# Performance work log

Measured on AMD Instinct MI355X. Metric: run time of the kernel, lower is better.

## Reference

```python
import jax, jax.numpy as jnp
import numpy as np

D_K = 64
D_MODEL = 1024
SEQ = 4096
BATCH = 4


def setup_inputs() -> dict:
    key = jax.random.key(0)
    ks = jax.random.split(key, 7)
    s = 1.0 / np.sqrt(D_MODEL)
    return {
        "x": jax.random.normal(ks[0], (BATCH, SEQ, D_MODEL), dtype=jnp.float32),
        "wq": jax.random.uniform(ks[1], (D_K, D_MODEL), jnp.float32, -s, s),
        "bq": jax.random.uniform(ks[2], (D_K,), jnp.float32, -s, s),
        "wk": jax.random.uniform(ks[3], (D_K, D_MODEL), jnp.float32, -s, s),
        "bk": jax.random.uniform(ks[4], (D_K,), jnp.float32, -s, s),
        "wv": jax.random.uniform(ks[5], (D_K, D_MODEL), jnp.float32, -s, s),
        "bv": jax.random.uniform(ks[6], (D_K,), jnp.float32, -s, s),
    }


def reference(x, wq, bq, wk, bk, wv, bv):
    # q,k,v: [B,T,d_k]
    q = jnp.einsum('btc,dc->btd', x, wq) + bq
    k = jnp.einsum('btc,dc->btd', x, wk) + bk
    v = jnp.einsum('btc,dc->btd', x, wv) + bv
    scale = 1.0 / np.sqrt(D_K).astype(np.float32)
    scores = jnp.einsum('bqd,bkd->bqk', q, k) * scale  # [B,T,T]
    T = x.shape[1]
    causal = jnp.tril(jnp.ones((T, T), dtype=bool))
    scores = jnp.where(causal, scores, -jnp.inf)
    sm = jax.nn.softmax(scores, axis=-1)
    return jnp.einsum('bqk,bkd->bqd', sm, v)
```

## Files before the change

kernel.cpp:

```cpp
#include <hip/hip_runtime.h>

typedef __attribute__((ext_vector_type(8))) short short8;
typedef __attribute__((ext_vector_type(4))) float f32x4;

#define D_KV   64
#define SEQ    4096
#define NBATCH 4
#define DMODEL 1024

static __device__ __forceinline__ unsigned short f32_to_bf16(float f) {
  unsigned u = __builtin_bit_cast(unsigned, f);
  u = (u + 0x7FFFu + ((u >> 16) & 1u)) >> 16;
  return (unsigned short)u;
}

__global__ __launch_bounds__(256) void xfrag_kernel(
    const float* __restrict__ x, unsigned short* __restrict__ xfrag) {
  __shared__ unsigned short lt[16 * 1024];
  const int tid = threadIdx.x;
  const long T = blockIdx.x;
  {
    const int row = tid >> 4, seg = tid & 15;
    const float* src = x + (T * 16 + row) * DMODEL + seg * 64;
    unsigned short* dst = lt + row * 1024 + seg * 64;
#pragma unroll
    for (int j = 0; j < 8; ++j) {
      const f32x4 f0 = *reinterpret_cast<const f32x4*>(src + j * 8);
      const f32x4 f1 = *reinterpret_cast<const f32x4*>(src + j * 8 + 4);
      short8 s;
#pragma unroll
      for (int q = 0; q < 4; ++q) {
        s[q] = (short)f32_to_bf16(f0[q]);
        s[4 + q] = (short)f32_to_bf16(f1[q]);
      }
      *reinterpret_cast<short8*>(dst + j * 8) = s;
    }
  }
  __syncthreads();
  unsigned short* dst = xfrag + T * 16384;
#pragma unroll
  for (int i = 0; i < 8; ++i) {
    const int slot = i * 256 + tid;
    const int lane2 = slot & 63, ks = slot >> 6;
    const short8 v = *reinterpret_cast<const short8*>(
        lt + (lane2 & 15) * 1024 + ks * 32 + (lane2 >> 4) * 8);
    *reinterpret_cast<short8*>(dst + slot * 8) = v;
  }
}

__global__ __launch_bounds__(256) void wcvt_kernel(
    const float* __restrict__ wq, const float* __restrict__ wk,
    const float* __restrict__ wv, unsigned short* __restrict__ wfrag) {
  const int fid = blockIdx.x * 256 + threadIdx.x;
  const int nt = fid >> 11, ks = (fid >> 6) & 31, lane = fid & 63;
  const int l16 = lane & 15, lq = lane >> 4;
  const float* w = (nt < 4) ? wq : (nt < 8) ? wk : wv;
  const float* src = w + ((nt & 3) * 16 + l16) * DMODEL + ks * 32 + lq * 8;
  short8 v;
#pragma unroll
  for (int j = 0; j < 8; ++j) v[j] = (short)f32_to_bf16(src[j]);
  *reinterpret_cast<short8*>(wfrag + (long)fid * 8) = v;
}

__global__ __launch_bounds__(256, 2) void qkv_proj_kernel(
    const unsigned short* __restrict__ xfrag,
    const unsigned short* __restrict__ wfrag,
    const float* __restrict__ bq, const float* __restrict__ bk,
    const float* __restrict__ bv,
    unsigned short* __restrict__ Qf, unsigned short* __restrict__ Kf,
    unsigned short* __restrict__ Vf) {
  const int tid = threadIdx.x, lane = tid & 63, wave = tid >> 6;
  const int l16 = lane & 15, lq = lane >> 4;
  const long T = blockIdx.x;

  const unsigned short* abase = xfrag + T * 16384 + lane * 8;
  const unsigned short* wbase = wfrag + (long)(3 * wave) * 16384 + lane * 8;

  f32x4 acc[3];
#pragma unroll
  for (int i = 0; i < 3; ++i) acc[i] = (f32x4){0.f, 0.f, 0.f, 0.f};

#pragma unroll
  for (int ck = 0; ck < 8; ++ck) {
    short8 a[4], bw[12];
#pragma unroll
    for (int kc = 0; kc < 4; ++kc)
      a[kc] = *reinterpret_cast<const short8*>(abase + (ck * 4 + kc) * 512);
#pragma unroll
    for (int j = 0; j < 12; ++j)
      bw[j] = *reinterpret_cast<const short8*>(
          wbase + (long)(j >> 2) * 16384 + (ck * 4 + (j & 3)) * 512);
#pragma unroll
    for (int kc = 0; kc < 4; ++kc)
#pragma unroll
      for (int i = 0; i < 3; ++i)
        acc[i] = __builtin_amdgcn_mfma_f32_16x16x32_bf16(
            a[kc], bw[i * 4 + kc], acc[i], 0, 0, 0);
  }

#pragma unroll
  for (int i = 0; i < 3; ++i) {
    const int nt = 3 * wave + i;
    const int mat = nt >> 2;
    const int dcol = ((nt & 3) << 4) | l16;
    const float bias = (mat == 0 ? bq : mat == 1 ? bk : bv)[dcol];
    const int c = dcol >> 5, lqp = (dcol >> 3) & 3, jj = dcol & 7;
#pragma unroll
    for (int rr = 0; rr < 4; ++rr) {
      const long t = T * 16 + lq * 4 + rr;
      const float sum = acc[i][rr] + bias;
      if (mat == 0) {
        Qf[(((t >> 4) * 2 + c) * 64 + lqp * 16 + (t & 15)) * 8 + jj] =
            f32_to_bf16(sum * 0.125f);
      } else if (mat == 1) {
        Kf[((((t >> 6) * 4 + ((t >> 4) & 3)) * 2 + c) * 64 + lqp * 16 +
            (t & 15)) * 8 + jj] = f32_to_bf16(sum);
      } else {
        Vf[((((t >> 6) * 4 + (dcol >> 4)) * 2 + ((t >> 5) & 1)) * 64 +
            ((t >> 3) & 3) * 16 + (dcol & 15)) * 8 + (t & 7)] =
            f32_to_bf16(sum);
      }
    }
  }
}

__global__ __launch_bounds__(256) void attn_kernel(
    const unsigned short* __restrict__ Qf, const unsigned short* __restrict__ Kf,
    const unsigned short* __restrict__ Vf, float* __restrict__ out) {
  __shared__ __align__(16) unsigned short p_lds[4][16][72];
  __shared__ __align__(16) float lds_o[4][16][68];
  __shared__ float lds_ml[4][16][2];
  __shared__ float lds_gl[16];

  const int tid = threadIdx.x;
  const int lane = tid & 63;
  const int wave = tid >> 6;
  const int l16 = lane & 15, lq = lane >> 4;
  const int b = blockIdx.y;
  const int tile = 255 - blockIdx.x;
  const int qbase = tile * 16;
  const long qrow = (long)b * SEQ + qbase;

  short8 qf[2];
#pragma unroll
  for (int c = 0; c < 2; ++c)
    qf[c] = *reinterpret_cast<const short8*>(
        Qf + ((qrow >> 4) * 2 + c) * 512 + lane * 8);

  f32x4 o[4];
#pragma unroll
  for (int dt = 0; dt < 4; ++dt) o[dt] = (f32x4){0.f, 0.f, 0.f, 0.f};
  float m = -INFINITY, ell = 0.f;

  const long ktile0 = (long)b * 64;
  const int nkv = qbase / 64 + 1;
  for (int kt = wave; kt < nkv; kt += 4) {
    const int kvbase = kt * 64;
    const unsigned short* kb = Kf + (ktile0 + kt) * 4096 + lane * 8;
    const unsigned short* vb = Vf + (ktile0 + kt) * 4096 + lane * 8;
    f32x4 s[4];
#pragma unroll
    for (int ct = 0; ct < 4; ++ct) s[ct] = (f32x4){0.f, 0.f, 0.f, 0.f};
#pragma unroll
    for (int ct = 0; ct < 4; ++ct)
#pragma unroll
      for (int c = 0; c < 2; ++c) {
        short8 kf = *reinterpret_cast<const short8*>(kb + (ct * 2 + c) * 512);
        s[ct] = __builtin_amdgcn_mfma_f32_16x16x32_bf16(kf, qf[c], s[ct], 0, 0, 0);
      }
    if (kt == nkv - 1) {
      const int qg = qbase + l16;
#pragma unroll
      for (int ct = 0; ct < 4; ++ct)
#pragma unroll
        for (int r = 0; r < 4; ++r)
          if (kvbase + ct * 16 + lq * 4 + r > qg) s[ct][r] = -INFINITY;
    }
    float mx = -INFINITY;
#pragma unroll
    for (int ct = 0; ct < 4; ++ct)
#pragma unroll
      for (int r = 0; r < 4; ++r) mx = fmaxf(mx, s[ct][r]);
    mx = fmaxf(mx, __shfl_xor(mx, 16, 64));
    mx = fmaxf(mx, __shfl_xor(mx, 32, 64));
    const float nm = fmaxf(m, mx);
    const float alpha = __expf(m - nm);
    float rs = 0.f;
#pragma unroll
    for (int ct = 0; ct < 4; ++ct)
#pragma unroll
      for (int r = 0; r < 4; ++r) {
        const float p = __expf(s[ct][r] - nm);
        s[ct][r] = p;
        rs += p;
      }
    rs += __shfl_xor(rs, 16, 64);
    rs += __shfl_xor(rs, 32, 64);
    ell = ell * alpha + rs;
    m = nm;
#pragma unroll
    for (int dt = 0; dt < 4; ++dt) o[dt] *= alpha;
#pragma unroll
    for (int ct = 0; ct < 4; ++ct)
#pragma unroll
      for (int r = 0; r < 4; ++r)
        p_lds[wave][l16][ct * 16 + lq * 4 + r] = f32_to_bf16(s[ct][r]);
    short8 pf[2];
#pragma unroll
    for (int c = 0; c < 2; ++c)
      pf[c] = *reinterpret_cast<const short8*>(&p_lds[wave][l16][c * 32 + lq * 8]);
#pragma unroll
    for (int dt = 0; dt < 4; ++dt)
#pragma unroll
      for (int c = 0; c < 2; ++c) {
        short8 vf = *reinterpret_cast<const short8*>(vb + (dt * 2 + c) * 512);
        o[dt] = __builtin_amdgcn_mfma_f32_16x16x32_bf16(vf, pf[c], o[dt], 0, 0, 0);
      }
  }

  if (lane < 16) {
    lds_ml[wave][l16][0] = m;
    lds_ml[wave][l16][1] = ell;
  }
  __syncthreads();
  const float m0 = lds_ml[0][l16][0], m1 = lds_ml[1][l16][0];
  const float m2 = lds_ml[2][l16][0], m3 = lds_ml[3][l16][0];
  const float g = fmaxf(fmaxf(m0, m1), fmaxf(m2, m3));
  const float gl = lds_ml[0][l16][1] * __expf(m0 - g) +
                   lds_ml[1][l16][1] * __expf(m1 - g) +
                   lds_ml[2][l16][1] * __expf(m2 - g) +
                   lds_ml[3][l16][1] * __expf(m3 - g);
  const float myscale = __expf(m - g);
  if (wave == 0 && lane < 16) lds_gl[l16] = gl;
#pragma unroll
  for (int dt = 0; dt < 4; ++dt)
#pragma unroll
    for (int r = 0; r < 4; ++r)
      lds_o[wave][l16][dt * 16 + lq * 4 + r] = o[dt][r] * myscale;
  __syncthreads();
#pragma unroll
  for (int j = 0; j < 4; ++j) {
    const int e = tid + 256 * j;
    const int row = e >> 6, col = e & 63;
    const float sum = lds_o[0][row][col] + lds_o[1][row][col] +
                      lds_o[2][row][col] + lds_o[3][row][col];
    out[(qrow + row) * D_KV + col] = sum / lds_gl[row];
  }
}

extern "C" void kernel_launch(void* const* d_in, const int* in_sizes, int n_in,
                              void* d_out, int out_size, void* d_ws, size_t ws_size,
                              hipStream_t stream) {
  const float* x  = (const float*)d_in[0];
  const float* wq = (const float*)d_in[1];
  const float* bq = (const float*)d_in[2];
  const float* wk = (const float*)d_in[3];
  const float* bk = (const float*)d_in[4];
  const float* wv = (const float*)d_in[5];
  const float* bv = (const float*)d_in[6];
  float* out = (float*)d_out;

  unsigned short* ws    = (unsigned short*)d_ws;
  unsigned short* wfrag = ws;
  unsigned short* Qf    = ws + 196608;
  unsigned short* Kf    = Qf + 1048576;
  unsigned short* Vf    = Kf + 1048576;
  unsigned short* xfrag = Vf + 1048576;

  xfrag_kernel<<<1024, 256, 0, stream>>>(x, xfrag);
  wcvt_kernel<<<96, 256, 0, stream>>>(wq, wk, wv, wfrag);
  qkv_proj_kernel<<<1024, 256, 0, stream>>>(xfrag, wfrag, bq, bk, bv, Qf, Kf, Vf);
  dim3 ag(256, NBATCH);
  attn_kernel<<<ag, 256, 0, stream>>>(Qf, Kf, Vf, out);
}
```

Baseline: 75.45 us.

## Reuse weight fragments across two row tiles and widen attention split-K to 8 waves

The QKV projection now has each wave compute two 16-row tiles with the same loaded weight fragments. This halves weight-fragment reloads per output and quarters the grid to 256 blocks of 512 threads. The attention kernel goes from 4 to 8 waves per query tile, each taking every eighth KV tile, with an 8-way LDS merge of the softmax statistics and partial outputs. This targets the causal load imbalance and gives more parallelism per block, at the cost of more registers, more LDS, and fewer projection blocks to fill the device.

```diff
diff --git a/kernel.cpp b/kernel.cpp
--- a/kernel.cpp
+++ b/kernel.cpp
@@ -62,7 +62,7 @@
   *reinterpret_cast<short8*>(wfrag + (long)fid * 8) = v;
 }
 
-__global__ __launch_bounds__(256, 2) void qkv_proj_kernel(
+__global__ __launch_bounds__(512, 1) void qkv_proj_kernel(
     const unsigned short* __restrict__ xfrag,
     const unsigned short* __restrict__ wfrag,
     const float* __restrict__ bq, const float* __restrict__ bk,
@@ -71,21 +71,27 @@
     unsigned short* __restrict__ Vf) {
   const int tid = threadIdx.x, lane = tid & 63, wave = tid >> 6;
   const int l16 = lane & 15, lq = lane >> 4;
-  const long T = blockIdx.x;
-
-  const unsigned short* abase = xfrag + T * 16384 + lane * 8;
-  const unsigned short* wbase = wfrag + (long)(3 * wave) * 16384 + lane * 8;
-
-  f32x4 acc[3];
-#pragma unroll
-  for (int i = 0; i < 3; ++i) acc[i] = (f32x4){0.f, 0.f, 0.f, 0.f};
+  const int trio = wave & 3;
+  const long T0 = (long)blockIdx.x * 4 + (wave >> 2) * 2;
+
+  const unsigned short* a0 = xfrag + T0 * 16384 + lane * 8;
+  const unsigned short* a1 = xfrag + (T0 + 1) * 16384 + lane * 8;
+  const unsigned short* wbase = wfrag + (long)(3 * trio) * 16384 + lane * 8;
+
+  f32x4 acc[3][2];
+#pragma unroll
+  for (int i = 0; i < 3; ++i)
+#pragma unroll
+    for (int p = 0; p < 2; ++p) acc[i][p] = (f32x4){0.f, 0.f, 0.f, 0.f};
 
 #pragma unroll
   for (int ck = 0; ck < 8; ++ck) {
-    short8 a[4], bw[12];
-#pragma unroll
-    for (int kc = 0; kc < 4; ++kc)
-      a[kc] = *reinterpret_cast<const short8*>(abase + (ck * 4 + kc) * 512);
+    short8 a[4][2], bw[12];
+#pragma unroll
+    for (int kc = 0; kc < 4; ++kc) {
+      a[kc][0] = *reinterpret_cast<const short8*>(a0 + (ck * 4 + kc) * 512);
+      a[kc][1] = *reinterpret_cast<const short8*>(a1 + (ck * 4 + kc) * 512);
+    }
 #pragma unroll
     for (int j = 0; j < 12; ++j)
       bw[j] = *reinterpret_cast<const short8*>(
@@ -93,43 +99,48 @@
 #pragma unroll
     for (int kc = 0; kc < 4; ++kc)
 #pragma unroll
-      for (int i = 0; i < 3; ++i)
-        acc[i] = __builtin_amdgcn_mfma_f32_16x16x32_bf16(
-            a[kc], bw[i * 4 + kc], acc[i], 0, 0, 0);
+      for (int i = 0; i < 3; ++i) {
+        acc[i][0] = __builtin_amdgcn_mfma_f32_16x16x32_bf16(
+            a[kc][0], bw[i * 4 + kc], acc[i][0], 0, 0, 0);
+        acc[i][1] = __builtin_amdgcn_mfma_f32_16x16x32_bf16(
+            a[kc][1], bw[i * 4 + kc], acc[i][1], 0, 0, 0);
+      }
   }
 
 #pragma unroll
   for (int i = 0; i < 3; ++i) {
-    const int nt = 3 * wave + i;
+    const int nt = 3 * trio + i;
     const int mat = nt >> 2;
     const int dcol = ((nt & 3) << 4) | l16;
     const float bias = (mat == 0 ? bq : mat == 1 ? bk : bv)[dcol];
     const int c = dcol >> 5, lqp = (dcol >> 3) & 3, jj = dcol & 7;
 #pragma unroll
-    for (int rr = 0; rr < 4; ++rr) {
-      const long t = T * 16 + lq * 4 + rr;
-      const float sum = acc[i][rr] + bias;
-      if (mat == 0) {
-        Qf[(((t >> 4) * 2 + c) * 64 + lqp * 16 + (t & 15)) * 8 + jj] =
-            f32_to_bf16(sum * 0.125f);
-      } else if (mat == 1) {
-        Kf[((((t >> 6) * 4 + ((t >> 4) & 3)) * 2 + c) * 64 + lqp * 16 +
-            (t & 15)) * 8 + jj] = f32_to_bf16(sum);
-      } else {
-        Vf[((((t >> 6) * 4 + (dcol >> 4)) * 2 + ((t >> 5) & 1)) * 64 +
-            ((t >> 3) & 3) * 16 + (dcol & 15)) * 8 + (t & 7)] =
-            f32_to_bf16(sum);
-      }
-    }
-  }
-}
-
-__global__ __launch_bounds__(256) void attn_kernel(
+    for (int p = 0; p < 2; ++p)
+#pragma unroll
+      for (int rr = 0; rr < 4; ++rr) {
+        const long t = (T0 + p) * 16 + lq * 4 + rr;
+        const float sum = acc[i][p][rr] + bias;
+        if (mat == 0) {
+          Qf[(((t >> 4) * 2 + c) * 64 + lqp * 16 + (t & 15)) * 8 + jj] =
+              f32_to_bf16(sum * 0.125f);
+        } else if (mat == 1) {
+          Kf[((((t >> 6) * 4 + ((t >> 4) & 3)) * 2 + c) * 64 + lqp * 16 +
+              (t & 15)) * 8 + jj] = f32_to_bf16(sum);
+        } else {
+          Vf[((((t >> 6) * 4 + (dcol >> 4)) * 2 + ((t >> 5) & 1)) * 64 +
+              ((t >> 3) & 3) * 16 + (dcol & 15)) * 8 + (t & 7)] =
+              f32_to_bf16(sum);
+        }
+      }
+  }
+}
+
+__global__ __launch_bounds__(512) void attn_kernel(
     const unsigned short* __restrict__ Qf, const unsigned short* __restrict__ Kf,
     const unsigned short* __restrict__ Vf, float* __restrict__ out) {
-  __shared__ __align__(16) unsigned short p_lds[4][16][72];
-  __shared__ __align__(16) float lds_o[4][16][68];
-  __shared__ float lds_ml[4][16][2];
+  __shared__ __align__(16) unsigned short p_lds[8][16][72];
+  __shared__ __align__(16) float lds_o[8][16][68];
+  __shared__ float lds_ml[8][16][2];
   __shared__ float lds_gl[16];
 
   const int tid = threadIdx.x;
@@ -154,7 +165,7 @@
 
   const long ktile0 = (long)b * 64;
   const int nkv = qbase / 64 + 1;
-  for (int kt = wave; kt < nkv; kt += 4) {
+  for (int kt = wave; kt < nkv; kt += 8) {
     const int kvbase = kt * 64;
     const unsigned short* kb = Kf + (ktile0 + kt) * 4096 + lane * 8;
     const unsigned short* vb = Vf + (ktile0 + kt) * 4096 + lane * 8;
@@ -223,13 +234,13 @@
     lds_ml[wave][l16][1] = ell;
   }
   __syncthreads();
-  const float m0 = lds_ml[0][l16][0], m1 = lds_ml[1][l16][0];
-  const float m2 = lds_ml[2][l16][0], m3 = lds_ml[3][l16][0];
-  const float g = fmaxf(fmaxf(m0, m1), fmaxf(m2, m3));
-  const float gl = lds_ml[0][l16][1] * __expf(m0 - g) +
-                   lds_ml[1][l16][1] * __expf(m1 - g) +
-                   lds_ml[2][l16][1] * __expf(m2 - g) +
-                   lds_ml[3][l16][1] * __expf(m3 - g);
+  float g = -INFINITY;
+#pragma unroll
+  for (int w2 = 0; w2 < 8; ++w2) g = fmaxf(g, lds_ml[w2][l16][0]);
+  float gl = 0.f;
+#pragma unroll
+  for (int w2 = 0; w2 < 8; ++w2)
+    gl += lds_ml[w2][l16][1] * __expf(lds_ml[w2][l16][0] - g);
   const float myscale = __expf(m - g);
   if (wave == 0 && lane < 16) lds_gl[l16] = gl;
 #pragma unroll
@@ -239,11 +250,12 @@
       lds_o[wave][l16][dt * 16 + lq * 4 + r] = o[dt][r] * myscale;
   __syncthreads();
 #pragma unroll
-  for (int j = 0; j < 4; ++j) {
-    const int e = tid + 256 * j;
+  for (int j = 0; j < 2; ++j) {
+    const int e = tid + 512 * j;
     const int row = e >> 6, col = e & 63;
-    const float sum = lds_o[0][row][col] + lds_o[1][row][col] +
-                      lds_o[2][row][col] + lds_o[3][row][col];
+    float sum = 0.f;
+#pragma unroll
+    for (int w2 = 0; w2 < 8; ++w2) sum += lds_o[w2][row][col];
     out[(qrow + row) * D_KV + col] = sum / lds_gl[row];
   }
 }
@@ -269,7 +281,7 @@
 
   xfrag_kernel<<<1024, 256, 0, stream>>>(x, xfrag);
   wcvt_kernel<<<96, 256, 0, stream>>>(wq, wk, wv, wfrag);
-  qkv_proj_kernel<<<1024, 256, 0, stream>>>(xfrag, wfrag, bq, bk, bv, Qf, Kf, Vf);
+  qkv_proj_kernel<<<256, 512, 0, stream>>>(xfrag, wfrag, bq, bk, bv, Qf, Kf, Vf);
   dim3 ag(256, NBATCH);
-  attn_kernel<<<ag, 256, 0, stream>>>(Qf, Kf, Vf, out);
-}
+  attn_kernel<<<ag, 512, 0, stream>>>(Qf, Kf, Vf, out);
+}
```

New measurement: 72.43 us. -4.0%, faster.
